# Optimization experiments

Hardware: AMD Instinct MI355X
Metric: run time of the kernel (lower is better)

Reference implementation:

```python
import jax, jax.numpy as jnp
import numpy as np

N_NODES = 100000
N_EDGES = 1600000
D_IN, D_H, D_OUT = 128, 64, 32


def _linear_init(key, out_dim, in_dim):
    # torch.nn.Linear default init: U(-1/sqrt(in), 1/sqrt(in))
    bound = 1.0 / np.sqrt(in_dim)
    return jax.random.uniform(key, (out_dim, in_dim), jnp.float32, -bound, bound)


def setup_inputs() -> dict:
    key = jax.random.key(0)
    ks = jax.random.split(key, 8)
    x = jax.random.normal(ks[0], (N_NODES, D_IN), dtype=jnp.float32)
    edge_index = jax.random.randint(ks[1], (2, N_EDGES), 0, N_NODES, dtype=jnp.int64)
    return {
        "x": x,
        "edge_index": edge_index,
        # SAGEConv layer 1: lin_l (neighbor agg, with bias), lin_r (root, no bias)
        "W1_l": _linear_init(ks[2], D_H, D_IN),
        "b1": jnp.zeros((D_H,), jnp.float32),
        "W1_r": _linear_init(ks[3], D_H, D_IN),
        # SAGEConv layer 2
        "W2_l": _linear_init(ks[4], D_OUT, D_H),
        "b2": jnp.zeros((D_OUT,), jnp.float32),
        "W2_r": _linear_init(ks[5], D_OUT, D_H),
    }


def _sage_conv(x, src, dst, W_l, b_l, W_r):
    """PyG SAGEConv with mean aggregation: lin_l(mean_{j in N(i)} x_j) + lin_r(x_i)."""
    n = x.shape[0]
    # scatter-mean of source features onto destination nodes
    agg = jax.ops.segment_sum(x[src], dst, num_segments=n)          # [N, d]
    deg = jax.ops.segment_sum(jnp.ones_like(dst, dtype=x.dtype), dst, num_segments=n)
    mean = agg / jnp.maximum(deg, 1.0)[:, None]
    return mean @ W_l.T + b_l + x @ W_r.T


def reference(x, edge_index, W1_l, b1, W1_r, W2_l, b2, W2_r):
    src, dst = edge_index[0], edge_index[1]
    h = _sage_conv(x, src, dst, W1_l, b1, W1_r)
    h = jax.nn.relu(h)
    # dropout p=0.5 is identity in eval mode
    return _sage_conv(h, src, dst, W2_l, b2, W2_r)
```

## Files before the change

kernel.cpp:

```cpp
#include <hip/hip_runtime.h>


namespace {
constexpr int N = 100000;
constexpr int E = 1600000;
constexpr int NBLK = (N + 255) / 256;
constexpr int NT16 = N / 16;
constexpr int NCHUNK = 64;
constexpr int CHUNK_N = 1600;
constexpr int CAP = 28000;
constexpr int PA_BLOCKS = 256;
constexpr int PER_BLK = E / PA_BLOCKS;
}

using bf16x8 = __attribute__((ext_vector_type(8))) short;
using f32x4  = __attribute__((ext_vector_type(4))) float;

__device__ __forceinline__ short f2bf(float f) {
    unsigned u = __builtin_bit_cast(unsigned, f);
    u += 0x7FFFu + ((u >> 16) & 1u);
    return (short)(u >> 16);
}

__device__ __forceinline__ float bf2f(unsigned short u) {
    return __builtin_bit_cast(float, (unsigned)u << 16);
}

__device__ __forceinline__ bf16x8 load_frag8(const float* __restrict__ p) {
    const float4* p4 = (const float4*)p;
    float4 f0 = p4[0], f1 = p4[1];
    bf16x8 r;
    r[0] = f2bf(f0.x); r[1] = f2bf(f0.y); r[2] = f2bf(f0.z); r[3] = f2bf(f0.w);
    r[4] = f2bf(f1.x); r[5] = f2bf(f1.y); r[6] = f2bf(f1.z); r[7] = f2bf(f1.w);
    return r;
}


__global__ __launch_bounds__(256) void detect_dtype(const int* __restrict__ raw,
                                                    int* __restrict__ flag,
                                                    int* __restrict__ bcur) {
    if (threadIdx.x < NCHUNK) bcur[threadIdx.x] = 0;
    int any = 0;
#pragma unroll
    for (int k = 0; k < 64; ++k) {
        int i = threadIdx.x + k * 256;
        any |= raw[2 * i + 1];
    }
    unsigned long long b = __ballot(any != 0);
    __shared__ int acc[4];
    int w = threadIdx.x >> 6;
    if ((threadIdx.x & 63) == 0) acc[w] = (b != 0ULL) ? 1 : 0;
    __syncthreads();
    if (threadIdx.x == 0) *flag = acc[0] | acc[1] | acc[2] | acc[3];
}

__global__ __launch_bounds__(256) void bucket_edges(
        const int* __restrict__ raw, const int* __restrict__ flag,
        int* __restrict__ bcur, int2* __restrict__ bucket) {
    __shared__ int cnt[NCHUNK];
    __shared__ int res[NCHUNK];
    if (threadIdx.x < NCHUNK) cnt[threadIdx.x] = 0;
    __syncthreads();
    const int is32 = *flag;
    const int e0 = blockIdx.x * PER_BLK;
    for (int i = threadIdx.x; i < PER_BLK; i += 256) {
        int e = e0 + i;
        int d = is32 ? raw[E + e] : raw[2 * ((long long)E + e)];
        atomicAdd(&cnt[d / CHUNK_N], 1);
    }
    __syncthreads();
    if (threadIdx.x < NCHUNK) {
        res[threadIdx.x] = atomicAdd(&bcur[threadIdx.x], cnt[threadIdx.x]);
        cnt[threadIdx.x] = 0;
    }
    __syncthreads();
    for (int i = threadIdx.x; i < PER_BLK; i += 256) {
        int e = e0 + i;
        int d, s;
        if (is32) { d = raw[E + e]; s = raw[e]; }
        else      { d = raw[2 * ((long long)E + e)]; s = raw[2 * (long long)e]; }
        int c = d / CHUNK_N;
        int pos = res[c] + atomicAdd(&cnt[c], 1);
        if (pos < CAP) bucket[(size_t)c * CAP + pos] = make_int2(s, d);
    }
}

__global__ __launch_bounds__(1024) void count2(
        const int* __restrict__ bcur, const int2* __restrict__ bucket,
        int* __restrict__ counts) {
    __shared__ int scnt[CHUNK_N];
    const int chunk = blockIdx.x;
    const int lo = chunk * CHUNK_N;
    for (int i = threadIdx.x; i < CHUNK_N; i += 1024) scnt[i] = 0;
    __syncthreads();
    int n = bcur[chunk]; if (n > CAP) n = CAP;
    const int2* b = bucket + (size_t)chunk * CAP;
    for (int i = threadIdx.x; i < n; i += 1024)
        atomicAdd(&scnt[b[i].y - lo], 1);
    __syncthreads();
    const int lim = N - lo;
    for (int i = threadIdx.x; i < CHUNK_N; i += 1024)
        if (i < lim) counts[lo + i] = scnt[i];
}

__global__ __launch_bounds__(256) void scan1(const int* __restrict__ counts,
                                             int* __restrict__ rowstart,
                                             int* __restrict__ bsum) {
    __shared__ int tmp[256];
    int t = threadIdx.x;
    int i = blockIdx.x * 256 + t;
    int v = (i < N) ? counts[i] : 0;
    tmp[t] = v;
    __syncthreads();
#pragma unroll
    for (int off = 1; off < 256; off <<= 1) {
        int a = (t >= off) ? tmp[t - off] : 0;
        __syncthreads();
        tmp[t] += a;
        __syncthreads();
    }
    if (i < N) rowstart[i] = tmp[t] - v;
    if (t == 255) bsum[blockIdx.x] = tmp[255];
}

__global__ __launch_bounds__(512) void scan2(int* __restrict__ bsum) {
    __shared__ int tmp[512];
    int t = threadIdx.x;
    int v = (t < NBLK) ? bsum[t] : 0;
    tmp[t] = v;
    __syncthreads();
#pragma unroll
    for (int off = 1; off < 512; off <<= 1) {
        int a = (t >= off) ? tmp[t - off] : 0;
        __syncthreads();
        tmp[t] += a;
        __syncthreads();
    }
    if (t < NBLK) bsum[t] = tmp[t] - v;
}

__global__ void scan3(int* __restrict__ rowstart, const int* __restrict__ bsum) {
    int i = blockIdx.x * blockDim.x + threadIdx.x;
    if (i < N) rowstart[i] += bsum[i >> 8];
    if (i == 0) rowstart[N] = E;
}

__global__ __launch_bounds__(1024) void fill2(
        const int* __restrict__ bcur, const int2* __restrict__ bucket,
        const int* __restrict__ rowstart, int* __restrict__ csr) {
    __shared__ int scur[CHUNK_N];
    const int chunk = blockIdx.x;
    const int lo = chunk * CHUNK_N;
    const int lim = N - lo;
    for (int i = threadIdx.x; i < CHUNK_N; i += 1024)
        scur[i] = (i < lim) ? rowstart[lo + i] : 0;
    __syncthreads();
    int n = bcur[chunk]; if (n > CAP) n = CAP;
    const int2* b = bucket + (size_t)chunk * CAP;
    for (int i = threadIdx.x; i < n; i += 1024) {
        int2 sd = b[i];
        int pos = atomicAdd(&scur[sd.y - lo], 1);
        csr[pos] = sd.x;
    }
}

__global__ __launch_bounds__(256) void transform1_mfma(
        const float* __restrict__ x, const float* __restrict__ W1l,
        const float* __restrict__ W1r, unsigned short* __restrict__ z1b,
        float* __restrict__ r1) {
    const int lane = threadIdx.x & 63;
    const int gw = blockIdx.x * 4 + (threadIdx.x >> 6);
    const int q = gw & 1;
    const int r16 = lane & 15;
    const int kgrp = lane >> 4;

    bf16x8 wf[2][2][4];
#pragma unroll
    for (int m = 0; m < 2; ++m) {
        const float* W = m ? W1r : W1l;
#pragma unroll
        for (int c = 0; c < 2; ++c) {
            const float* pw = W + (size_t)(q * 32 + c * 16 + r16) * 128 + kgrp * 8;
#pragma unroll
            for (int kb = 0; kb < 4; ++kb)
                wf[m][c][kb] = load_frag8(pw + kb * 32);
        }
    }

    const int stride = (gridDim.x * 4) >> 1;
    for (int t = gw >> 1; t < NT16; t += stride) {
        const float* px = x + ((size_t)t * 16 + r16) * 128 + kgrp * 8;
        bf16x8 af[4];
#pragma unroll
        for (int kb = 0; kb < 4; ++kb) af[kb] = load_frag8(px + kb * 32);

        f32x4 a00 = {0.f,0.f,0.f,0.f}, a01 = {0.f,0.f,0.f,0.f};
        f32x4 a10 = {0.f,0.f,0.f,0.f}, a11 = {0.f,0.f,0.f,0.f};
#pragma unroll
        for (int kb = 0; kb < 4; ++kb) {
            a00 = __builtin_amdgcn_mfma_f32_16x16x32_bf16(af[kb], wf[0][0][kb], a00, 0, 0, 0);
            a01 = __builtin_amdgcn_mfma_f32_16x16x32_bf16(af[kb], wf[0][1][kb], a01, 0, 0, 0);
            a10 = __builtin_amdgcn_mfma_f32_16x16x32_bf16(af[kb], wf[1][0][kb], a10, 0, 0, 0);
            a11 = __builtin_amdgcn_mfma_f32_16x16x32_bf16(af[kb], wf[1][1][kb], a11, 0, 0, 0);
        }
#pragma unroll
        for (int i = 0; i < 4; ++i) {
            size_t row = (size_t)t * 16 + kgrp * 4 + i;
            z1b[row * 64 + q * 32 +  0 + r16] = (unsigned short)f2bf(a00[i]);
            z1b[row * 64 + q * 32 + 16 + r16] = (unsigned short)f2bf(a01[i]);
            r1[row * 64 + q * 32 +  0 + r16] = a10[i];
            r1[row * 64 + q * 32 + 16 + r16] = a11[i];
        }
    }
}

__global__ __launch_bounds__(256) void transform2_mfma(
        const float* __restrict__ h, const float* __restrict__ W2l,
        const float* __restrict__ W2r, unsigned short* __restrict__ z2b,
        float* __restrict__ r2) {
    const int lane = threadIdx.x & 63;
    const int gw = blockIdx.x * 4 + (threadIdx.x >> 6);
    const int r16 = lane & 15;
    const int kgrp = lane >> 4;

    bf16x8 wf[2][2][2];
#pragma unroll
    for (int m = 0; m < 2; ++m) {
        const float* W = m ? W2r : W2l;
#pragma unroll
        for (int c = 0; c < 2; ++c) {
            const float* pw = W + (size_t)(c * 16 + r16) * 64 + kgrp * 8;
#pragma unroll
            for (int kb = 0; kb < 2; ++kb)
                wf[m][c][kb] = load_frag8(pw + kb * 32);
        }
    }

    for (int t = gw; t < NT16; t += gridDim.x * 4) {
        const float* ph = h + ((size_t)t * 16 + r16) * 64 + kgrp * 8;
        bf16x8 af[2];
        af[0] = load_frag8(ph);
        af[1] = load_frag8(ph + 32);

        f32x4 a00 = {0.f,0.f,0.f,0.f}, a01 = {0.f,0.f,0.f,0.f};
        f32x4 a10 = {0.f,0.f,0.f,0.f}, a11 = {0.f,0.f,0.f,0.f};
#pragma unroll
        for (int kb = 0; kb < 2; ++kb) {
            a00 = __builtin_amdgcn_mfma_f32_16x16x32_bf16(af[kb], wf[0][0][kb], a00, 0, 0, 0);
            a01 = __builtin_amdgcn_mfma_f32_16x16x32_bf16(af[kb], wf[0][1][kb], a01, 0, 0, 0);
            a10 = __builtin_amdgcn_mfma_f32_16x16x32_bf16(af[kb], wf[1][0][kb], a10, 0, 0, 0);
            a11 = __builtin_amdgcn_mfma_f32_16x16x32_bf16(af[kb], wf[1][1][kb], a11, 0, 0, 0);
        }
#pragma unroll
        for (int i = 0; i < 4; ++i) {
            size_t row = (size_t)t * 16 + kgrp * 4 + i;
            z2b[row * 32 +  0 + r16] = (unsigned short)f2bf(a00[i]);
            z2b[row * 32 + 16 + r16] = (unsigned short)f2bf(a01[i]);
            r2[row * 32 +  0 + r16] = a10[i];
            r2[row * 32 + 16 + r16] = a11[i];
        }
    }
}


__global__ __launch_bounds__(256) void agg1_fused(
        const int* __restrict__ rowstart, const int* __restrict__ csr,
        const unsigned short* __restrict__ z1b, const float* __restrict__ r1,
        const float* __restrict__ b1, float* __restrict__ h) {
    const int n = blockIdx.x * 4 + (threadIdx.x >> 6);
    if (n >= N) return;
    const int j = threadIdx.x & 63;
    const int beg = rowstart[n], end = rowstart[n + 1];
    float s = 0.f;
    int p = beg;
    for (; p + 8 <= end; p += 8) {
        int c0 = csr[p],     c1 = csr[p + 1], c2 = csr[p + 2], c3 = csr[p + 3];
        int c4 = csr[p + 4], c5 = csr[p + 5], c6 = csr[p + 6], c7 = csr[p + 7];
        s += bf2f(z1b[(size_t)c0 * 64 + j]) + bf2f(z1b[(size_t)c1 * 64 + j])
           + bf2f(z1b[(size_t)c2 * 64 + j]) + bf2f(z1b[(size_t)c3 * 64 + j])
           + bf2f(z1b[(size_t)c4 * 64 + j]) + bf2f(z1b[(size_t)c5 * 64 + j])
           + bf2f(z1b[(size_t)c6 * 64 + j]) + bf2f(z1b[(size_t)c7 * 64 + j]);
    }
    for (; p < end; ++p) s += bf2f(z1b[(size_t)csr[p] * 64 + j]);
    float m = (end > beg) ? s / (float)(end - beg) : 0.f;
    size_t o = (size_t)n * 64 + j;
    h[o] = fmaxf(m + b1[j] + r1[o], 0.f);
}

__global__ __launch_bounds__(256) void agg2_fused(
        const int* __restrict__ rowstart, const int* __restrict__ csr,
        const unsigned short* __restrict__ z2b, const float* __restrict__ r2,
        const float* __restrict__ b2, float* __restrict__ out) {
    const int wid = blockIdx.x * 4 + (threadIdx.x >> 6);
    const int n = wid * 2 + ((threadIdx.x >> 5) & 1);
    if (n >= N) return;
    const int j = threadIdx.x & 31;
    const int beg = rowstart[n], end = rowstart[n + 1];
    float s = 0.f;
    int p = beg;
    for (; p + 4 <= end; p += 4) {
        int c0 = csr[p], c1 = csr[p + 1], c2 = csr[p + 2], c3 = csr[p + 3];
        s += bf2f(z2b[(size_t)c0 * 32 + j]) + bf2f(z2b[(size_t)c1 * 32 + j])
           + bf2f(z2b[(size_t)c2 * 32 + j]) + bf2f(z2b[(size_t)c3 * 32 + j]);
    }
    for (; p < end; ++p) s += bf2f(z2b[(size_t)csr[p] * 32 + j]);
    float m = (end > beg) ? s / (float)(end - beg) : 0.f;
    size_t o = (size_t)n * 32 + j;
    out[o] = m + b2[j] + r2[o];
}


extern "C" void kernel_launch(void* const* d_in, const int* in_sizes, int n_in,
                              void* d_out, int out_size, void* d_ws, size_t ws_size,
                              hipStream_t stream) {
    const float* x    = (const float*)d_in[0];
    const int*   raw  = (const int*)d_in[1];
    const float* W1l  = (const float*)d_in[2];
    const float* b1   = (const float*)d_in[3];
    const float* W1r  = (const float*)d_in[4];
    const float* W2l  = (const float*)d_in[5];
    const float* b2   = (const float*)d_in[6];
    const float* W2r  = (const float*)d_in[7];
    float* out = (float*)d_out;

    char* wsb = (char*)d_ws;
    unsigned short* z1b = (unsigned short*)wsb;
    unsigned short* z2b = (unsigned short*)wsb;
    float* r1 = (float*)(wsb + 16 * 1024 * 1024);
    float* r2 = (float*)(wsb + 16 * 1024 * 1024);
    float* h  = (float*)(wsb + 48 * 1024 * 1024);
    int2* bucket = (int2*)(wsb + 48 * 1024 * 1024);

    int* ibase    = (int*)(wsb + 80 * 1024 * 1024);
    int* counts   = ibase;
    int* rowstart = ibase + N;
    int* bsum     = ibase + 2 * N + 1;
    int* csr      = ibase + 2 * N + 1 + 512;
    int* flag     = csr + E;
    int* bcur     = flag + 1;

    detect_dtype<<<1, 256, 0, stream>>>(raw, flag, bcur);
    bucket_edges<<<PA_BLOCKS, 256, 0, stream>>>(raw, flag, bcur, bucket);
    count2<<<NCHUNK, 1024, 0, stream>>>(bcur, bucket, counts);
    scan1<<<NBLK, 256, 0, stream>>>(counts, rowstart, bsum);
    scan2<<<1, 512, 0, stream>>>(bsum);
    scan3<<<NBLK, 256, 0, stream>>>(rowstart, bsum);
    fill2<<<NCHUNK, 1024, 0, stream>>>(bcur, bucket, rowstart, csr);

    transform1_mfma<<<1024, 256, 0, stream>>>(x, W1l, W1r, z1b, r1);
    agg1_fused<<<(N + 3) / 4, 256, 0, stream>>>(rowstart, csr, z1b, r1, b1, h);

    transform2_mfma<<<1024, 256, 0, stream>>>(h, W2l, W2r, z2b, r2);
    agg2_fused<<<(N + 7) / 8, 256, 0, stream>>>(rowstart, csr, z2b, r2, b2, out);
}
```

Measured before the change: 224.5 us.

## Gather packed bf16 pairs and split edges across wave sub-groups in aggregation

Measured after the change: 215.7 us. 3.9% less time.

```diff
diff --git a/kernel.cpp b/kernel.cpp
--- a/kernel.cpp
+++ b/kernel.cpp
@@ -22,10 +22,6 @@
     return (short)(u >> 16);
 }
 
-__device__ __forceinline__ float bf2f(unsigned short u) {
-    return __builtin_bit_cast(float, (unsigned)u << 16);
-}
-
 __device__ __forceinline__ bf16x8 load_frag8(const float* __restrict__ p) {
     const float4* p4 = (const float4*)p;
     float4 f0 = p4[0], f1 = p4[1];
@@ -33,6 +29,13 @@
     r[0] = f2bf(f0.x); r[1] = f2bf(f0.y); r[2] = f2bf(f0.z); r[3] = f2bf(f0.w);
     r[4] = f2bf(f1.x); r[5] = f2bf(f1.y); r[6] = f2bf(f1.z); r[7] = f2bf(f1.w);
     return r;
+}
+
+__device__ __forceinline__ float pk_lo(unsigned u) {
+    return __builtin_bit_cast(float, u << 16);
+}
+__device__ __forceinline__ float pk_hi(unsigned u) {
+    return __builtin_bit_cast(float, u & 0xFFFF0000u);
 }
 
 
@@ -265,48 +268,98 @@
 
 __global__ __launch_bounds__(256) void agg1_fused(
         const int* __restrict__ rowstart, const int* __restrict__ csr,
-        const unsigned short* __restrict__ z1b, const float* __restrict__ r1,
+        const unsigned* __restrict__ z1w, const float* __restrict__ r1,
         const float* __restrict__ b1, float* __restrict__ h) {
     const int n = blockIdx.x * 4 + (threadIdx.x >> 6);
     if (n >= N) return;
-    const int j = threadIdx.x & 63;
+    const int lane = threadIdx.x & 63;
+    const int half = lane >> 5;
+    const int fl = lane & 31;
     const int beg = rowstart[n], end = rowstart[n + 1];
-    float s = 0.f;
+    float alo = 0.f, ahi = 0.f;
     int p = beg;
     for (; p + 8 <= end; p += 8) {
-        int c0 = csr[p],     c1 = csr[p + 1], c2 = csr[p + 2], c3 = csr[p + 3];
-        int c4 = csr[p + 4], c5 = csr[p + 5], c6 = csr[p + 6], c7 = csr[p + 7];
-        s += bf2f(z1b[(size_t)c0 * 64 + j]) + bf2f(z1b[(size_t)c1 * 64 + j])
-           + bf2f(z1b[(size_t)c2 * 64 + j]) + bf2f(z1b[(size_t)c3 * 64 + j])
-           + bf2f(z1b[(size_t)c4 * 64 + j]) + bf2f(z1b[(size_t)c5 * 64 + j])
-           + bf2f(z1b[(size_t)c6 * 64 + j]) + bf2f(z1b[(size_t)c7 * 64 + j]);
-    }
-    for (; p < end; ++p) s += bf2f(z1b[(size_t)csr[p] * 64 + j]);
-    float m = (end > beg) ? s / (float)(end - beg) : 0.f;
-    size_t o = (size_t)n * 64 + j;
-    h[o] = fmaxf(m + b1[j] + r1[o], 0.f);
+        int c0 = csr[p + 0 + half], c1 = csr[p + 2 + half];
+        int c2 = csr[p + 4 + half], c3 = csr[p + 6 + half];
+        unsigned u0 = z1w[(size_t)c0 * 32 + fl];
+        unsigned u1 = z1w[(size_t)c1 * 32 + fl];
+        unsigned u2 = z1w[(size_t)c2 * 32 + fl];
+        unsigned u3 = z1w[(size_t)c3 * 32 + fl];
+        alo += pk_lo(u0) + pk_lo(u1) + pk_lo(u2) + pk_lo(u3);
+        ahi += pk_hi(u0) + pk_hi(u1) + pk_hi(u2) + pk_hi(u3);
+    }
+    for (; p + 2 <= end; p += 2) {
+        int c = csr[p + half];
+        unsigned u = z1w[(size_t)c * 32 + fl];
+        alo += pk_lo(u);
+        ahi += pk_hi(u);
+    }
+    if (p < end && half == 0) {
+        int c = csr[p];
+        unsigned u = z1w[(size_t)c * 32 + fl];
+        alo += pk_lo(u);
+        ahi += pk_hi(u);
+    }
+    alo += __shfl_xor(alo, 32, 64);
+    ahi += __shfl_xor(ahi, 32, 64);
+    if (half == 0) {
+        float inv = (end > beg) ? 1.0f / (float)(end - beg) : 0.f;
+        float2 rv = ((const float2*)r1)[(size_t)n * 32 + fl];
+        float2 bv = ((const float2*)b1)[fl];
+        float2 o;
+        o.x = fmaxf(alo * inv + bv.x + rv.x, 0.f);
+        o.y = fmaxf(ahi * inv + bv.y + rv.y, 0.f);
+        ((float2*)h)[(size_t)n * 32 + fl] = o;
+    }
 }
 
 __global__ __launch_bounds__(256) void agg2_fused(
         const int* __restrict__ rowstart, const int* __restrict__ csr,
-        const unsigned short* __restrict__ z2b, const float* __restrict__ r2,
+        const unsigned* __restrict__ z2w, const float* __restrict__ r2,
         const float* __restrict__ b2, float* __restrict__ out) {
-    const int wid = blockIdx.x * 4 + (threadIdx.x >> 6);
-    const int n = wid * 2 + ((threadIdx.x >> 5) & 1);
+    const int n = blockIdx.x * 4 + (threadIdx.x >> 6);
     if (n >= N) return;
-    const int j = threadIdx.x & 31;
+    const int lane = threadIdx.x & 63;
+    const int quad = lane >> 4;
+    const int fl = lane & 15;
     const int beg = rowstart[n], end = rowstart[n + 1];
-    float s = 0.f;
+    float alo = 0.f, ahi = 0.f;
     int p = beg;
+    for (; p + 8 <= end; p += 8) {
+        int c0 = csr[p + quad], c1 = csr[p + 4 + quad];
+        unsigned u0 = z2w[(size_t)c0 * 16 + fl];
+        unsigned u1 = z2w[(size_t)c1 * 16 + fl];
+        alo += pk_lo(u0) + pk_lo(u1);
+        ahi += pk_hi(u0) + pk_hi(u1);
+    }
     for (; p + 4 <= end; p += 4) {
-        int c0 = csr[p], c1 = csr[p + 1], c2 = csr[p + 2], c3 = csr[p + 3];
-        s += bf2f(z2b[(size_t)c0 * 32 + j]) + bf2f(z2b[(size_t)c1 * 32 + j])
-           + bf2f(z2b[(size_t)c2 * 32 + j]) + bf2f(z2b[(size_t)c3 * 32 + j]);
-    }
-    for (; p < end; ++p) s += bf2f(z2b[(size_t)csr[p] * 32 + j]);
-    float m = (end > beg) ? s / (float)(end - beg) : 0.f;
-    size_t o = (size_t)n * 32 + j;
-    out[o] = m + b2[j] + r2[o];
+        int c = csr[p + quad];
+        unsigned u = z2w[(size_t)c * 16 + fl];
+        alo += pk_lo(u);
+        ahi += pk_hi(u);
+    }
+    if (p < end) {
+        int r = end - p;
+        if (quad < r) {
+            int c = csr[p + quad];
+            unsigned u = z2w[(size_t)c * 16 + fl];
+            alo += pk_lo(u);
+            ahi += pk_hi(u);
+        }
+    }
+    alo += __shfl_xor(alo, 16, 64);
+    ahi += __shfl_xor(ahi, 16, 64);
+    alo += __shfl_xor(alo, 32, 64);
+    ahi += __shfl_xor(ahi, 32, 64);
+    if (lane < 16) {
+        float inv = (end > beg) ? 1.0f / (float)(end - beg) : 0.f;
+        float2 rv = ((const float2*)r2)[(size_t)n * 16 + fl];
+        float2 bv = ((const float2*)b2)[fl];
+        float2 o;
+        o.x = alo * inv + bv.x + rv.x;
+        o.y = ahi * inv + bv.y + rv.y;
+        ((float2*)out)[(size_t)n * 16 + fl] = o;
+    }
 }
 
 
@@ -348,8 +401,8 @@
     fill2<<<NCHUNK, 1024, 0, stream>>>(bcur, bucket, rowstart, csr);
 
     transform1_mfma<<<1024, 256, 0, stream>>>(x, W1l, W1r, z1b, r1);
-    agg1_fused<<<(N + 3) / 4, 256, 0, stream>>>(rowstart, csr, z1b, r1, b1, h);
+    agg1_fused<<<(N + 3) / 4, 256, 0, stream>>>(rowstart, csr, (const unsigned*)z1b, r1, b1, h);
 
     transform2_mfma<<<1024, 256, 0, stream>>>(h, W2l, W2r, z2b, r2);
-    agg2_fused<<<(N + 7) / 8, 256, 0, stream>>>(rowstart, csr, z2b, r2, b2, out);
-}
+    agg2_fused<<<(N + 3) / 4, 256, 0, stream>>>(rowstart, csr, (const unsigned*)z2b, r2, b2, out);
+}
```

## Vectorize neighbor gathers over multiple edges per wave and store hidden layer as bf16

Applied to the files above, without the earlier changes.

After: 206.5 us. 8.0% less time.

```diff
diff --git a/kernel.cpp b/kernel.cpp
--- a/kernel.cpp
+++ b/kernel.cpp
@@ -16,14 +16,10 @@
 using bf16x8 = __attribute__((ext_vector_type(8))) short;
 using f32x4  = __attribute__((ext_vector_type(4))) float;
 
-__device__ __forceinline__ short f2bf(float f) {
+__device__ __forceinline__ unsigned short f2bf(float f) {
     unsigned u = __builtin_bit_cast(unsigned, f);
     u += 0x7FFFu + ((u >> 16) & 1u);
-    return (short)(u >> 16);
-}
-
-__device__ __forceinline__ float bf2f(unsigned short u) {
-    return __builtin_bit_cast(float, (unsigned)u << 16);
+    return (unsigned short)(u >> 16);
 }
 
 __device__ __forceinline__ bf16x8 load_frag8(const float* __restrict__ p) {
@@ -33,6 +29,16 @@
     r[0] = f2bf(f0.x); r[1] = f2bf(f0.y); r[2] = f2bf(f0.z); r[3] = f2bf(f0.w);
     r[4] = f2bf(f1.x); r[5] = f2bf(f1.y); r[6] = f2bf(f1.z); r[7] = f2bf(f1.w);
     return r;
+}
+
+__device__ __forceinline__ float pk_lo(unsigned u) {
+    return __builtin_bit_cast(float, u << 16);
+}
+__device__ __forceinline__ float pk_hi(unsigned u) {
+    return __builtin_bit_cast(float, u & 0xFFFF0000u);
+}
+__device__ __forceinline__ unsigned pk2(float a, float b) {
+    return (unsigned)f2bf(a) | ((unsigned)f2bf(b) << 16);
 }
 
 
@@ -206,8 +212,8 @@
 #pragma unroll
         for (int i = 0; i < 4; ++i) {
             size_t row = (size_t)t * 16 + kgrp * 4 + i;
-            z1b[row * 64 + q * 32 +  0 + r16] = (unsigned short)f2bf(a00[i]);
-            z1b[row * 64 + q * 32 + 16 + r16] = (unsigned short)f2bf(a01[i]);
+            z1b[row * 64 + q * 32 +  0 + r16] = f2bf(a00[i]);
+            z1b[row * 64 + q * 32 + 16 + r16] = f2bf(a01[i]);
             r1[row * 64 + q * 32 +  0 + r16] = a10[i];
             r1[row * 64 + q * 32 + 16 + r16] = a11[i];
         }
@@ -215,7 +221,7 @@
 }
 
 __global__ __launch_bounds__(256) void transform2_mfma(
-        const float* __restrict__ h, const float* __restrict__ W2l,
+        const unsigned short* __restrict__ hb, const float* __restrict__ W2l,
         const float* __restrict__ W2r, unsigned short* __restrict__ z2b,
         float* __restrict__ r2) {
     const int lane = threadIdx.x & 63;
@@ -237,10 +243,10 @@
     }
 
     for (int t = gw; t < NT16; t += gridDim.x * 4) {
-        const float* ph = h + ((size_t)t * 16 + r16) * 64 + kgrp * 8;
+        const unsigned short* ph = hb + ((size_t)t * 16 + r16) * 64 + kgrp * 8;
         bf16x8 af[2];
-        af[0] = load_frag8(ph);
-        af[1] = load_frag8(ph + 32);
+        af[0] = *(const bf16x8*)(ph);
+        af[1] = *(const bf16x8*)(ph + 32);
 
         f32x4 a00 = {0.f,0.f,0.f,0.f}, a01 = {0.f,0.f,0.f,0.f};
         f32x4 a10 = {0.f,0.f,0.f,0.f}, a11 = {0.f,0.f,0.f,0.f};
@@ -254,59 +260,113 @@
 #pragma unroll
         for (int i = 0; i < 4; ++i) {
             size_t row = (size_t)t * 16 + kgrp * 4 + i;
-            z2b[row * 32 +  0 + r16] = (unsigned short)f2bf(a00[i]);
-            z2b[row * 32 + 16 + r16] = (unsigned short)f2bf(a01[i]);
+            z2b[row * 32 +  0 + r16] = f2bf(a00[i]);
+            z2b[row * 32 + 16 + r16] = f2bf(a01[i]);
             r2[row * 32 +  0 + r16] = a10[i];
             r2[row * 32 + 16 + r16] = a11[i];
         }
     }
 }
 
-
 __global__ __launch_bounds__(256) void agg1_fused(
         const int* __restrict__ rowstart, const int* __restrict__ csr,
-        const unsigned short* __restrict__ z1b, const float* __restrict__ r1,
-        const float* __restrict__ b1, float* __restrict__ h) {
+        const uint2* __restrict__ z1d, const float* __restrict__ r1,
+        const float* __restrict__ b1, uint2* __restrict__ hb) {
     const int n = blockIdx.x * 4 + (threadIdx.x >> 6);
     if (n >= N) return;
-    const int j = threadIdx.x & 63;
+    const int lane = threadIdx.x & 63;
+    const int quad = lane >> 4;
+    const int fl = lane & 15;
     const int beg = rowstart[n], end = rowstart[n + 1];
-    float s = 0.f;
+    float a0 = 0.f, a1 = 0.f, a2 = 0.f, a3 = 0.f;
     int p = beg;
     for (; p + 8 <= end; p += 8) {
-        int c0 = csr[p],     c1 = csr[p + 1], c2 = csr[p + 2], c3 = csr[p + 3];
-        int c4 = csr[p + 4], c5 = csr[p + 5], c6 = csr[p + 6], c7 = csr[p + 7];
-        s += bf2f(z1b[(size_t)c0 * 64 + j]) + bf2f(z1b[(size_t)c1 * 64 + j])
-           + bf2f(z1b[(size_t)c2 * 64 + j]) + bf2f(z1b[(size_t)c3 * 64 + j])
-           + bf2f(z1b[(size_t)c4 * 64 + j]) + bf2f(z1b[(size_t)c5 * 64 + j])
-           + bf2f(z1b[(size_t)c6 * 64 + j]) + bf2f(z1b[(size_t)c7 * 64 + j]);
-    }
-    for (; p < end; ++p) s += bf2f(z1b[(size_t)csr[p] * 64 + j]);
-    float m = (end > beg) ? s / (float)(end - beg) : 0.f;
-    size_t o = (size_t)n * 64 + j;
-    h[o] = fmaxf(m + b1[j] + r1[o], 0.f);
+        int c0 = csr[p + quad], c1 = csr[p + 4 + quad];
+        uint2 u0 = z1d[(size_t)c0 * 16 + fl];
+        uint2 u1 = z1d[(size_t)c1 * 16 + fl];
+        a0 += pk_lo(u0.x) + pk_lo(u1.x);
+        a1 += pk_hi(u0.x) + pk_hi(u1.x);
+        a2 += pk_lo(u0.y) + pk_lo(u1.y);
+        a3 += pk_hi(u0.y) + pk_hi(u1.y);
+    }
+    for (; p + 4 <= end; p += 4) {
+        int c = csr[p + quad];
+        uint2 u = z1d[(size_t)c * 16 + fl];
+        a0 += pk_lo(u.x); a1 += pk_hi(u.x);
+        a2 += pk_lo(u.y); a3 += pk_hi(u.y);
+    }
+    if (p < end) {
+        int rem = end - p;
+        if (quad < rem) {
+            int c = csr[p + quad];
+            uint2 u = z1d[(size_t)c * 16 + fl];
+            a0 += pk_lo(u.x); a1 += pk_hi(u.x);
+            a2 += pk_lo(u.y); a3 += pk_hi(u.y);
+        }
+    }
+    a0 += __shfl_xor(a0, 16, 64); a1 += __shfl_xor(a1, 16, 64);
+    a2 += __shfl_xor(a2, 16, 64); a3 += __shfl_xor(a3, 16, 64);
+    a0 += __shfl_xor(a0, 32, 64); a1 += __shfl_xor(a1, 32, 64);
+    a2 += __shfl_xor(a2, 32, 64); a3 += __shfl_xor(a3, 32, 64);
+    if (lane < 16) {
+        float inv = (end > beg) ? 1.0f / (float)(end - beg) : 0.f;
+        float4 rv = ((const float4*)r1)[(size_t)n * 16 + fl];
+        float4 bv = ((const float4*)b1)[fl];
+        float h0 = fmaxf(a0 * inv + bv.x + rv.x, 0.f);
+        float h1 = fmaxf(a1 * inv + bv.y + rv.y, 0.f);
+        float h2 = fmaxf(a2 * inv + bv.z + rv.z, 0.f);
+        float h3 = fmaxf(a3 * inv + bv.w + rv.w, 0.f);
+        uint2 o;
+        o.x = pk2(h0, h1);
+        o.y = pk2(h2, h3);
+        hb[(size_t)n * 16 + fl] = o;
+    }
 }
 
 __global__ __launch_bounds__(256) void agg2_fused(
         const int* __restrict__ rowstart, const int* __restrict__ csr,
-        const unsigned short* __restrict__ z2b, const float* __restrict__ r2,
+        const uint2* __restrict__ z2d, const float* __restrict__ r2,
         const float* __restrict__ b2, float* __restrict__ out) {
-    const int wid = blockIdx.x * 4 + (threadIdx.x >> 6);
-    const int n = wid * 2 + ((threadIdx.x >> 5) & 1);
+    const int n = blockIdx.x * 4 + (threadIdx.x >> 6);
     if (n >= N) return;
-    const int j = threadIdx.x & 31;
+    const int lane = threadIdx.x & 63;
+    const int oct = lane >> 3;
+    const int fl = lane & 7;
     const int beg = rowstart[n], end = rowstart[n + 1];
-    float s = 0.f;
+    float a0 = 0.f, a1 = 0.f, a2 = 0.f, a3 = 0.f;
     int p = beg;
-    for (; p + 4 <= end; p += 4) {
-        int c0 = csr[p], c1 = csr[p + 1], c2 = csr[p + 2], c3 = csr[p + 3];
-        s += bf2f(z2b[(size_t)c0 * 32 + j]) + bf2f(z2b[(size_t)c1 * 32 + j])
-           + bf2f(z2b[(size_t)c2 * 32 + j]) + bf2f(z2b[(size_t)c3 * 32 + j]);
-    }
-    for (; p < end; ++p) s += bf2f(z2b[(size_t)csr[p] * 32 + j]);
-    float m = (end > beg) ? s / (float)(end - beg) : 0.f;
-    size_t o = (size_t)n * 32 + j;
-    out[o] = m + b2[j] + r2[o];
+    for (; p + 8 <= end; p += 8) {
+        int c = csr[p + oct];
+        uint2 u = z2d[(size_t)c * 8 + fl];
+        a0 += pk_lo(u.x); a1 += pk_hi(u.x);
+        a2 += pk_lo(u.y); a3 += pk_hi(u.y);
+    }
+    if (p < end) {
+        int rem = end - p;
+        if (oct < rem) {
+            int c = csr[p + oct];
+            uint2 u = z2d[(size_t)c * 8 + fl];
+            a0 += pk_lo(u.x); a1 += pk_hi(u.x);
+            a2 += pk_lo(u.y); a3 += pk_hi(u.y);
+        }
+    }
+    a0 += __shfl_xor(a0, 8, 64);  a1 += __shfl_xor(a1, 8, 64);
+    a2 += __shfl_xor(a2, 8, 64);  a3 += __shfl_xor(a3, 8, 64);
+    a0 += __shfl_xor(a0, 16, 64); a1 += __shfl_xor(a1, 16, 64);
+    a2 += __shfl_xor(a2, 16, 64); a3 += __shfl_xor(a3, 16, 64);
+    a0 += __shfl_xor(a0, 32, 64); a1 += __shfl_xor(a1, 32, 64);
+    a2 += __shfl_xor(a2, 32, 64); a3 += __shfl_xor(a3, 32, 64);
+    if (lane < 8) {
+        float inv = (end > beg) ? 1.0f / (float)(end - beg) : 0.f;
+        float4 rv = ((const float4*)r2)[(size_t)n * 8 + fl];
+        float4 bv = ((const float4*)b2)[fl];
+        float4 o;
+        o.x = a0 * inv + bv.x + rv.x;
+        o.y = a1 * inv + bv.y + rv.y;
+        o.z = a2 * inv + bv.z + rv.z;
+        o.w = a3 * inv + bv.w + rv.w;
+        ((float4*)out)[(size_t)n * 8 + fl] = o;
+    }
 }
 
 
@@ -328,8 +388,8 @@
     unsigned short* z2b = (unsigned short*)wsb;
     float* r1 = (float*)(wsb + 16 * 1024 * 1024);
     float* r2 = (float*)(wsb + 16 * 1024 * 1024);
-    float* h  = (float*)(wsb + 48 * 1024 * 1024);
-    int2* bucket = (int2*)(wsb + 48 * 1024 * 1024);
+    unsigned short* hb = (unsigned short*)(wsb + 48 * 1024 * 1024);
+    int2* bucket = (int2*)(wsb + 64 * 1024 * 1024);
 
     int* ibase    = (int*)(wsb + 80 * 1024 * 1024);
     int* counts   = ibase;
@@ -348,8 +408,8 @@
     fill2<<<NCHUNK, 1024, 0, stream>>>(bcur, bucket, rowstart, csr);
 
     transform1_mfma<<<1024, 256, 0, stream>>>(x, W1l, W1r, z1b, r1);
-    agg1_fused<<<(N + 3) / 4, 256, 0, stream>>>(rowstart, csr, z1b, r1, b1, h);
-
-    transform2_mfma<<<1024, 256, 0, stream>>>(h, W2l, W2r, z2b, r2);
-    agg2_fused<<<(N + 7) / 8, 256, 0, stream>>>(rowstart, csr, z2b, r2, b2, out);
-}
+    agg1_fused<<<(N + 3) / 4, 256, 0, stream>>>(rowstart, csr, (const uint2*)z1b, r1, b1, (uint2*)hb);
+
+    transform2_mfma<<<1024, 256, 0, stream>>>(hb, W2l, W2r, z2b, r2);
+    agg2_fused<<<(N + 3) / 4, 256, 0, stream>>>(rowstart, csr, (const uint2*)z2b, r2, b2, out);
+}
```
